# Kernel tuning notes

Hardware: AMD Instinct MI355X
Metric: run time of the kernel (lower is better)

## Reference

```python
import jax, jax.numpy as jnp
import numpy as np

B, H, W, N, DX, DZ = 4, 64, 64, 4096, 2, 128
INIT_LS = 0.1


def setup_inputs() -> dict:
    key = jax.random.key(0)
    k1, k2, k3, k4 = jax.random.split(key, 4)
    xc_off_grid = jax.random.uniform(k1, (B, N, DX), dtype=jnp.float32)
    # regular grid coordinates in [0, 1]^2, broadcast over batch
    gy, gx = jnp.meshgrid(jnp.linspace(0.0, 1.0, H), jnp.linspace(0.0, 1.0, W), indexing="ij")
    xc_on_grid = jnp.broadcast_to(jnp.stack([gy, gx], axis=-1)[None], (B, H, W, DX)).astype(jnp.float32)
    zc_off_grid = jax.random.normal(k2, (B, N, DZ), dtype=jnp.float32)
    zc_on_grid = jax.random.normal(k3, (B, H, W, DZ), dtype=jnp.float32)
    # lengthscale_param = log(exp(init_lengthscale) - 1)  (inverse softplus)
    lengthscale_param = jnp.log(jnp.expm1(jnp.full((DX,), INIT_LS, dtype=jnp.float32)))
    return {
        "xc_off_grid": xc_off_grid,
        "xc_on_grid": xc_on_grid,
        "zc_off_grid": zc_off_grid,
        "zc_on_grid": zc_on_grid,
        "lengthscale_param": lengthscale_param,
        "ignore_on_grid": 0,
    }


def reference(xc_off_grid, xc_on_grid, zc_off_grid, zc_on_grid, lengthscale_param, ignore_on_grid):
    b = xc_on_grid.shape[0]
    grid_shape = xc_on_grid.shape[1:-1]
    dz = zc_off_grid.shape[-1]
    xg = xc_on_grid.reshape(b, -1, xc_on_grid.shape[-1])  # [b, m, dx]
    lengthscale = 1e-05 + jax.nn.softplus(lengthscale_param)  # [dx]
    # squared scaled distances: [b, m, n]
    diff = (xg[:, :, None, :] - xc_off_grid[:, None, :, :]) / lengthscale
    weights = jnp.exp(-0.5 * jnp.sum(diff * diff, axis=-1))  # [b, m, n]
    zc = jnp.einsum("bmn,bnd->bmd", weights, zc_off_grid)  # [b, m, dz]
    if not ignore_on_grid:
        zc = zc + zc_on_grid.reshape(b, -1, dz)
    return zc.reshape((b,) + grid_shape + (dz,))
```

## Files before the change

kernel.cpp:

```cpp
#include <hip/hip_runtime.h>

#define HH 64
#define WW 64
#define NN 4096
#define DZc 128
#define KS 8
#define BK 64
#define NKT (NN / KS / BK)
#define CELLS 2097152
#define WS_NEED (8ull * CELLS * 4ull)

typedef __fp16 v2fp16 __attribute__((ext_vector_type(2)));
typedef _Float16 v4h __attribute__((ext_vector_type(4)));
typedef _Float16 v8h __attribute__((ext_vector_type(8)));
typedef float v16f __attribute__((ext_vector_type(16)));

__device__ __forceinline__ unsigned pk16(float lo, float hi){
  union { v2fp16 h; unsigned u; } c;
  c.h = __builtin_amdgcn_cvt_pkrtz(lo, hi);
  return c.u;
}
__device__ __forceinline__ float fexp2(float x){ return __builtin_amdgcn_exp2f(x); }

__global__ void init_out_kernel(const float4* __restrict__ zc_on,
                                const int* __restrict__ ignore,
                                float4* __restrict__ out){
  int i = blockIdx.x * blockDim.x + threadIdx.x;
  float4 v = zc_on[i];
  if (ignore[0]) { v.x = 0.f; v.y = 0.f; v.z = 0.f; v.w = 0.f; }
  out[i] = v;
}

__global__ void reduce_kernel(const float4* __restrict__ part,
                              const float4* __restrict__ zc_on,
                              const int* __restrict__ ignore,
                              float4* __restrict__ out){
  int i = blockIdx.x * blockDim.x + threadIdx.x;
  float4 s = zc_on[i];
  if (ignore[0]) { s.x = 0.f; s.y = 0.f; s.z = 0.f; s.w = 0.f; }
  #pragma unroll
  for (int ks = 0; ks < KS; ++ks){
    float4 p = part[(size_t)ks * (CELLS / 4) + i];
    s.x += p.x; s.y += p.y; s.z += p.z; s.w += p.w;
  }
  out[i] = s;
}

__global__ __launch_bounds__(256, 2)
void setconv_gemm_kernel(const float* __restrict__ xc_off,
                         const float* __restrict__ xc_on,
                         const float* __restrict__ zc_off,
                         const float* __restrict__ lsp,
                         float* __restrict__ part,
                         float* __restrict__ out)
{
  __shared__ unsigned short zt[2][128][68];
  __shared__ unsigned short gt[2][40][68];

  const int tid = threadIdx.x;
  const int bid = blockIdx.x;
  const int ks  = bid >> 6;
  const int bm  = bid & 63;
  const int b   = bm >> 4;
  const int mt  = bm & 15;
  const int iy0 = (mt >> 3) * 32;
  const int ix0 = (mt & 7) * 8;
  const int nbase = ks * (NN / KS);

  const float lsy = 1e-5f + log1pf(expf(lsp[0]));
  const float lsx = 1e-5f + log1pf(expf(lsp[1]));
  const float LOG2E = 1.44269504088896340736f;
  const float ay = -0.5f * LOG2E / (lsy * lsy);
  const float ax = -0.5f * LOG2E / (lsx * lsx);

  const int gp = tid & 31;
  const int gr = tid >> 5;
  float gc[5], ga[5];
  #pragma unroll
  for (int i = 0; i < 5; ++i){
    int row = gr + 8 * i;
    if (row < 32){ gc[i] = xc_on[((b * HH + iy0 + row) * WW) * 2];        ga[i] = ay; }
    else         { gc[i] = xc_on[(b * HH * WW + ix0 + row - 32) * 2 + 1]; ga[i] = ax; }
  }

  const int zd  = (tid & 63) | (((tid >> 6) & 1) << 6);
  const int zkh = tid >> 7;

  const int lane = tid & 63;
  const int wv  = tid >> 6;
  const int l31 = lane & 31;
  const int lh  = lane >> 5;
  const int gxr = 32 + (l31 & 7);
  const int gyr = wv * 8 + (l31 >> 3);

  v16f acc[2][4];
  #pragma unroll
  for (int m = 0; m < 2; ++m)
    #pragma unroll
    for (int d = 0; d < 4; ++d)
      #pragma unroll
      for (int r = 0; r < 16; ++r)
        acc[m][d][r] = 0.f;

  const float* xb = xc_off + (size_t)b * NN * 2;
  const float* zb = zc_off + (size_t)b * NN * DZc;

  {
    const int n0 = nbase;
    float4 xq = *(const float4*)&xb[(size_t)(n0 + 2 * gp) * 2];
    unsigned* gw = (unsigned*)&gt[0][0][0];
    #pragma unroll
    for (int i = 0; i < 5; ++i){
      int row = gr + 8 * i;
      float s0 = (row < 32) ? xq.x : xq.y;
      float s1 = (row < 32) ? xq.z : xq.w;
      float d0 = gc[i] - s0, d1 = gc[i] - s1;
      gw[row * 34 + gp] = pk16(fexp2(ga[i] * d0 * d0), fexp2(ga[i] * d1 * d1));
    }
    float zv[32];
    #pragma unroll
    for (int i = 0; i < 32; ++i)
      zv[i] = zb[(size_t)(n0 + zkh * 32 + i) * DZc + zd];
    #pragma unroll
    for (int j = 0; j < 8; ++j){
      union { unsigned u[2]; double d; } w;
      w.u[0] = pk16(zv[4 * j],     zv[4 * j + 1]);
      w.u[1] = pk16(zv[4 * j + 2], zv[4 * j + 3]);
      *(double*)&zt[0][zd][zkh * 32 + 4 * j] = w.d;
    }
  }
  __syncthreads();

  #pragma unroll 1
  for (int kt = 0; kt < NKT; ++kt){
    const int buf  = kt & 1;
    const int nbuf = buf ^ 1;
    const bool have_next = (kt + 1 < NKT);
    const int n1 = nbase + (kt + 1) * BK;

    float zv[32];
    float4 xq_n = (float4){0.f, 0.f, 0.f, 0.f};
    if (have_next){
      #pragma unroll
      for (int i = 0; i < 32; ++i)
        zv[i] = zb[(size_t)(n1 + zkh * 32 + i) * DZc + zd];
      xq_n = *(const float4*)&xb[(size_t)(n1 + 2 * gp) * 2];
    }

    #pragma unroll
    for (int kstep = 0; kstep < 2; ++kstep){
      const int k0 = kstep * 16 + lh * 8;
      union { v4h h[2]; v8h v; } xu;
      xu.h[0] = *(const v4h*)&gt[buf][gxr][k0];
      xu.h[1] = *(const v4h*)&gt[buf][gxr][k0 + 4];
      v8h bfr[4];
      #pragma unroll
      for (int dtl = 0; dtl < 4; ++dtl){
        union { v4h h[2]; v8h v; } zu;
        zu.h[0] = *(const v4h*)&zt[buf][dtl * 32 + l31][k0];
        zu.h[1] = *(const v4h*)&zt[buf][dtl * 32 + l31][k0 + 4];
        bfr[dtl] = zu.v;
      }
      #pragma unroll
      for (int mtl = 0; mtl < 2; ++mtl){
        union { v4h h[2]; v8h v; } yu;
        yu.h[0] = *(const v4h*)&gt[buf][gyr + mtl * 4][k0];
        yu.h[1] = *(const v4h*)&gt[buf][gyr + mtl * 4][k0 + 4];
        v8h av = yu.v * xu.v;
        #pragma unroll
        for (int dtl = 0; dtl < 4; ++dtl)
          acc[mtl][dtl] = __builtin_amdgcn_mfma_f32_32x32x16_f16(av, bfr[dtl], acc[mtl][dtl], 0, 0, 0);
      }
    }

    if (have_next){
      #pragma unroll
      for (int j = 0; j < 8; ++j){
        union { unsigned u[2]; double d; } w;
        w.u[0] = pk16(zv[4 * j],     zv[4 * j + 1]);
        w.u[1] = pk16(zv[4 * j + 2], zv[4 * j + 3]);
        *(double*)&zt[nbuf][zd][zkh * 32 + 4 * j] = w.d;
      }
    }

    #pragma unroll
    for (int kstep = 2; kstep < 4; ++kstep){
      const int k0 = kstep * 16 + lh * 8;
      union { v4h h[2]; v8h v; } xu;
      xu.h[0] = *(const v4h*)&gt[buf][gxr][k0];
      xu.h[1] = *(const v4h*)&gt[buf][gxr][k0 + 4];
      v8h bfr[4];
      #pragma unroll
      for (int dtl = 0; dtl < 4; ++dtl){
        union { v4h h[2]; v8h v; } zu;
        zu.h[0] = *(const v4h*)&zt[buf][dtl * 32 + l31][k0];
        zu.h[1] = *(const v4h*)&zt[buf][dtl * 32 + l31][k0 + 4];
        bfr[dtl] = zu.v;
      }
      #pragma unroll
      for (int mtl = 0; mtl < 2; ++mtl){
        union { v4h h[2]; v8h v; } yu;
        yu.h[0] = *(const v4h*)&gt[buf][gyr + mtl * 4][k0];
        yu.h[1] = *(const v4h*)&gt[buf][gyr + mtl * 4][k0 + 4];
        v8h av = yu.v * xu.v;
        #pragma unroll
        for (int dtl = 0; dtl < 4; ++dtl)
          acc[mtl][dtl] = __builtin_amdgcn_mfma_f32_32x32x16_f16(av, bfr[dtl], acc[mtl][dtl], 0, 0, 0);
      }
    }

    if (have_next){
      unsigned* gw = (unsigned*)&gt[nbuf][0][0];
      #pragma unroll
      for (int i = 0; i < 5; ++i){
        int row = gr + 8 * i;
        float s0 = (row < 32) ? xq_n.x : xq_n.y;
        float s1 = (row < 32) ? xq_n.z : xq_n.w;
        float d0 = gc[i] - s0, d1 = gc[i] - s1;
        gw[row * 34 + gp] = pk16(fexp2(ga[i] * d0 * d0), fexp2(ga[i] * d1 * d1));
      }
    }
    __syncthreads();
  }

  if (part){
    float* pw = part + (size_t)ks * CELLS;
    #pragma unroll
    for (int mtl = 0; mtl < 2; ++mtl)
      #pragma unroll
      for (int dtl = 0; dtl < 4; ++dtl){
        const int d = dtl * 32 + l31;
        #pragma unroll
        for (int reg = 0; reg < 16; ++reg){
          const int row = (reg & 3) + 8 * (reg >> 2) + 4 * lh;
          const int m = wv * 64 + mtl * 32 + row;
          const int iy = iy0 + (m >> 3);
          const int ix = ix0 + (m & 7);
          pw[((b * HH + iy) * WW + ix) * DZc + d] = acc[mtl][dtl][reg];
        }
      }
  } else {
    #pragma unroll
    for (int mtl = 0; mtl < 2; ++mtl)
      #pragma unroll
      for (int dtl = 0; dtl < 4; ++dtl){
        const int d = dtl * 32 + l31;
        #pragma unroll
        for (int reg = 0; reg < 16; ++reg){
          const int row = (reg & 3) + 8 * (reg >> 2) + 4 * lh;
          const int m = wv * 64 + mtl * 32 + row;
          const int iy = iy0 + (m >> 3);
          const int ix = ix0 + (m & 7);
          unsafeAtomicAdd(&out[((b * HH + iy) * WW + ix) * DZc + d], acc[mtl][dtl][reg]);
        }
      }
  }
}

extern "C" void kernel_launch(void* const* d_in, const int* in_sizes, int n_in,
                              void* d_out, int out_size, void* d_ws, size_t ws_size,
                              hipStream_t stream){
  const float* xc_off = (const float*)d_in[0];
  const float* xc_on  = (const float*)d_in[1];
  const float* zc_off = (const float*)d_in[2];
  const float* zc_on  = (const float*)d_in[3];
  const float* lsp    = (const float*)d_in[4];
  const int*   ign    = (const int*)d_in[5];
  float* out = (float*)d_out;

  if (ws_size >= WS_NEED){
    float* part = (float*)d_ws;
    setconv_gemm_kernel<<<KS * 64, 256, 0, stream>>>(xc_off, xc_on, zc_off, lsp, part, out);
    reduce_kernel<<<CELLS / 4 / 256, 256, 0, stream>>>((const float4*)part, (const float4*)zc_on, ign, (float4*)out);
  } else {
    init_out_kernel<<<out_size / 1024, 256, 0, stream>>>((const float4*)zc_on, ign, (float4*)out);
    setconv_gemm_kernel<<<KS * 64, 256, 0, stream>>>(xc_off, xc_on, zc_off, lsp, nullptr, out);
  }
}
```

Measured before the change: 115.7 us.

## Store split-K partials in fp16 and widen LDS rows for 16-byte loads

The split-K partial sums are now written to the workspace as fp16 instead of fp32, which halves the write and read traffic between the GEMM kernel and the reduce kernel and halves the workspace requirement. The grid-weight LDS row stride is padded from 68 to 72 halves so that 8-half vector loads are 16-byte aligned and can be issued as single loads. The two k-step halves are merged into one loop, with the next tile's z store and weight compute moved after it. Rounding partial sums to fp16 loses precision in the reduction and could hurt accuracy, and moving the staging work after the MFMA loop reduces its interleaving with the math.

```diff
diff --git a/kernel.cpp b/kernel.cpp
--- a/kernel.cpp
+++ b/kernel.cpp
@@ -8,7 +8,7 @@
 #define BK 64
 #define NKT (NN / KS / BK)
 #define CELLS 2097152
-#define WS_NEED (8ull * CELLS * 4ull)
+#define WS_NEED (8ull * CELLS * 2ull)
 
 typedef __fp16 v2fp16 __attribute__((ext_vector_type(2)));
 typedef _Float16 v4h __attribute__((ext_vector_type(4)));
@@ -31,7 +31,7 @@
   out[i] = v;
 }
 
-__global__ void reduce_kernel(const float4* __restrict__ part,
+__global__ void reduce_kernel(const v4h* __restrict__ part,
                               const float4* __restrict__ zc_on,
                               const int* __restrict__ ignore,
                               float4* __restrict__ out){
@@ -40,8 +40,8 @@
   if (ignore[0]) { s.x = 0.f; s.y = 0.f; s.z = 0.f; s.w = 0.f; }
   #pragma unroll
   for (int ks = 0; ks < KS; ++ks){
-    float4 p = part[(size_t)ks * (CELLS / 4) + i];
-    s.x += p.x; s.y += p.y; s.z += p.z; s.w += p.w;
+    v4h p = part[(size_t)ks * (CELLS / 4) + i];
+    s.x += (float)p[0]; s.y += (float)p[1]; s.z += (float)p[2]; s.w += (float)p[3];
   }
   out[i] = s;
 }
@@ -51,11 +51,11 @@
                          const float* __restrict__ xc_on,
                          const float* __restrict__ zc_off,
                          const float* __restrict__ lsp,
-                         float* __restrict__ part,
+                         _Float16* __restrict__ part,
                          float* __restrict__ out)
 {
   __shared__ unsigned short zt[2][128][68];
-  __shared__ unsigned short gt[2][40][68];
+  __shared__ unsigned short gt[2][40][72];
 
   const int tid = threadIdx.x;
   const int bid = blockIdx.x;
@@ -115,7 +115,7 @@
       float s0 = (row < 32) ? xq.x : xq.y;
       float s1 = (row < 32) ? xq.z : xq.w;
       float d0 = gc[i] - s0, d1 = gc[i] - s1;
-      gw[row * 34 + gp] = pk16(fexp2(ga[i] * d0 * d0), fexp2(ga[i] * d1 * d1));
+      gw[row * 36 + gp] = pk16(fexp2(ga[i] * d0 * d0), fexp2(ga[i] * d1 * d1));
     }
     float zv[32];
     #pragma unroll
@@ -148,11 +148,9 @@
     }
 
     #pragma unroll
-    for (int kstep = 0; kstep < 2; ++kstep){
+    for (int kstep = 0; kstep < 4; ++kstep){
       const int k0 = kstep * 16 + lh * 8;
-      union { v4h h[2]; v8h v; } xu;
-      xu.h[0] = *(const v4h*)&gt[buf][gxr][k0];
-      xu.h[1] = *(const v4h*)&gt[buf][gxr][k0 + 4];
+      const v8h xu = *(const v8h*)&gt[buf][gxr][k0];
       v8h bfr[4];
       #pragma unroll
       for (int dtl = 0; dtl < 4; ++dtl){
@@ -163,10 +161,8 @@
       }
       #pragma unroll
       for (int mtl = 0; mtl < 2; ++mtl){
-        union { v4h h[2]; v8h v; } yu;
-        yu.h[0] = *(const v4h*)&gt[buf][gyr + mtl * 4][k0];
-        yu.h[1] = *(const v4h*)&gt[buf][gyr + mtl * 4][k0 + 4];
-        v8h av = yu.v * xu.v;
+        const v8h yu = *(const v8h*)&gt[buf][gyr + mtl * 4][k0];
+        v8h av = yu * xu;
         #pragma unroll
         for (int dtl = 0; dtl < 4; ++dtl)
           acc[mtl][dtl] = __builtin_amdgcn_mfma_f32_32x32x16_f16(av, bfr[dtl], acc[mtl][dtl], 0, 0, 0);
@@ -181,35 +177,6 @@
         w.u[1] = pk16(zv[4 * j + 2], zv[4 * j + 3]);
         *(double*)&zt[nbuf][zd][zkh * 32 + 4 * j] = w.d;
       }
-    }
-
-    #pragma unroll
-    for (int kstep = 2; kstep < 4; ++kstep){
-      const int k0 = kstep * 16 + lh * 8;
-      union { v4h h[2]; v8h v; } xu;
-      xu.h[0] = *(const v4h*)&gt[buf][gxr][k0];
-      xu.h[1] = *(const v4h*)&gt[buf][gxr][k0 + 4];
-      v8h bfr[4];
-      #pragma unroll
-      for (int dtl = 0; dtl < 4; ++dtl){
-        union { v4h h[2]; v8h v; } zu;
-        zu.h[0] = *(const v4h*)&zt[buf][dtl * 32 + l31][k0];
-        zu.h[1] = *(const v4h*)&zt[buf][dtl * 32 + l31][k0 + 4];
-        bfr[dtl] = zu.v;
-      }
-      #pragma unroll
-      for (int mtl = 0; mtl < 2; ++mtl){
-        union { v4h h[2]; v8h v; } yu;
-        yu.h[0] = *(const v4h*)&gt[buf][gyr + mtl * 4][k0];
-        yu.h[1] = *(const v4h*)&gt[buf][gyr + mtl * 4][k0 + 4];
-        v8h av = yu.v * xu.v;
-        #pragma unroll
-        for (int dtl = 0; dtl < 4; ++dtl)
-          acc[mtl][dtl] = __builtin_amdgcn_mfma_f32_32x32x16_f16(av, bfr[dtl], acc[mtl][dtl], 0, 0, 0);
-      }
-    }
-
-    if (have_next){
       unsigned* gw = (unsigned*)&gt[nbuf][0][0];
       #pragma unroll
       for (int i = 0; i < 5; ++i){
@@ -217,14 +184,14 @@
         float s0 = (row < 32) ? xq_n.x : xq_n.y;
         float s1 = (row < 32) ? xq_n.z : xq_n.w;
         float d0 = gc[i] - s0, d1 = gc[i] - s1;
-        gw[row * 34 + gp] = pk16(fexp2(ga[i] * d0 * d0), fexp2(ga[i] * d1 * d1));
+        gw[row * 36 + gp] = pk16(fexp2(ga[i] * d0 * d0), fexp2(ga[i] * d1 * d1));
       }
     }
     __syncthreads();
   }
 
   if (part){
-    float* pw = part + (size_t)ks * CELLS;
+    _Float16* pw = part + (size_t)ks * CELLS;
     #pragma unroll
     for (int mtl = 0; mtl < 2; ++mtl)
       #pragma unroll
@@ -236,7 +203,7 @@
           const int m = wv * 64 + mtl * 32 + row;
           const int iy = iy0 + (m >> 3);
           const int ix = ix0 + (m & 7);
-          pw[((b * HH + iy) * WW + ix) * DZc + d] = acc[mtl][dtl][reg];
+          pw[((b * HH + iy) * WW + ix) * DZc + d] = (_Float16)acc[mtl][dtl][reg];
         }
       }
   } else {
@@ -269,9 +236,9 @@
   float* out = (float*)d_out;
 
   if (ws_size >= WS_NEED){
-    float* part = (float*)d_ws;
+    _Float16* part = (_Float16*)d_ws;
     setconv_gemm_kernel<<<KS * 64, 256, 0, stream>>>(xc_off, xc_on, zc_off, lsp, part, out);
-    reduce_kernel<<<CELLS / 4 / 256, 256, 0, stream>>>((const float4*)part, (const float4*)zc_on, ign, (float4*)out);
+    reduce_kernel<<<CELLS / 4 / 256, 256, 0, stream>>>((const v4h*)part, (const float4*)zc_on, ign, (float4*)out);
   } else {
     init_out_kernel<<<out_size / 1024, 256, 0, stream>>>((const float4*)zc_on, ign, (float4*)out);
     setconv_gemm_kernel<<<KS * 64, 256, 0, stream>>>(xc_off, xc_on, zc_off, lsp, nullptr, out);
```

Measured after the change: 108.9 us. 1.06x faster.
